# Optimization experiments

Measured on AMD Instinct MI355X. Metric: run time of the kernel, lower is better.

The kernel has to match this reference:

```python
import jax, jax.numpy as jnp
import numpy as np

L = 1024
D = 512      # d_model
H = 256      # hidden


def setup_inputs() -> dict:
    key = jax.random.key(0)
    k1, k2, k3, k4, k5 = jax.random.split(key, 5)
    scale = 0.02
    return {
        "seq_feats": jax.random.normal(k1, (L, D), dtype=jnp.float32),
        "W1": jax.random.normal(k2, (H, 2 * D), dtype=jnp.float32) * scale,
        "b1": jax.random.normal(k3, (H,), dtype=jnp.float32) * scale,
        "W2": jax.random.normal(k4, (1, H), dtype=jnp.float32) * scale,
        "b2": jax.random.normal(k5, (1,), dtype=jnp.float32) * scale,
    }


def reference(seq_feats, W1, b1, W2, b2):
    # cat([a, b]) @ W1.T == a @ W1[:, :D].T + b @ W1[:, D:].T
    # so we never materialize the [L, L, 2D] concat tensor.
    d = seq_feats.shape[1]
    pa = seq_feats @ W1[:, :d].T          # [L, H] (row / i contribution)
    pb = seq_feats @ W1[:, d:].T          # [L, H] (col / j contribution)
    h = jax.nn.relu(pa[:, None, :] + pb[None, :, :] + b1)  # [L, L, H]
    scores = jnp.einsum("ijh,h->ij", h, W2[0]) + b2[0]      # [L, L]
    scores = (scores + scores.T) * 0.5
    return jax.nn.sigmoid(scores)
```

## Files before the change

kernel.cpp:

```cpp
#include <hip/hip_runtime.h>
#include <hip/hip_bf16.h>
#include <math.h>

#define LL 1024
#define DD 512
#define HH 256

typedef __attribute__((ext_vector_type(8))) short bf16x8;
typedef __attribute__((ext_vector_type(4))) float f32x4;


__device__ __forceinline__ ushort f2bf(float f) {
  __hip_bfloat16 h = __float2bfloat16(f);
  return *reinterpret_cast<ushort*>(&h);
}
__device__ __forceinline__ float bfu(ushort u) {
  return __uint_as_float(((unsigned int)u) << 16);
}

__global__ __launch_bounds__(256) void sp_convert(
    const float* __restrict__ S, const float* __restrict__ W1,
    ushort* __restrict__ Sb, ushort* __restrict__ Wb) {
  const int m = blockIdx.x * 256 + threadIdx.x;
  const int NS = (LL * DD) / 4;
  if (m < NS) {
    const float4 v = ((const float4*)S)[m];
    ushort4 o;
    o.x = f2bf(v.x); o.y = f2bf(v.y); o.z = f2bf(v.z); o.w = f2bf(v.w);
    ((ushort4*)Sb)[m] = o;
  } else {
    const int w  = m - NS;
    const int n  = w >> 7;
    const int kg = w & 127;
    const float4 v = *(const float4*)(W1 + (size_t)(n & 255) * 1024 +
                                      (n >> 8) * 512 + 4 * kg);
    ushort4 o;
    o.x = f2bf(v.x); o.y = f2bf(v.y); o.z = f2bf(v.z); o.w = f2bf(v.w);
    *(ushort4*)(Wb + (size_t)n * 512 + 4 * kg) = o;
  }
}

__global__ __launch_bounds__(256) void sp_mgemm(
    const ushort* __restrict__ Wb, const ushort* __restrict__ Sb,
    const float* __restrict__ b1, ushort* __restrict__ O) {
  const int tid  = threadIdx.x;
  const int lane = tid & 63;
  const int wv   = tid >> 6;
  const int i0   = blockIdx.x * 32 + (wv >> 1) * 16;
  const int n0   = blockIdx.y * 32 + (wv & 1) * 16;
  const int lr   = lane & 15;
  const int lg   = lane >> 4;

  const ushort* ap = Wb + (size_t)(n0 + lr) * 512 + lg * 8;
  const ushort* bp = Sb + (size_t)(i0 + lr) * 512 + lg * 8;

  f32x4 acc = {0.f, 0.f, 0.f, 0.f};
  #pragma unroll
  for (int ks = 0; ks < 512; ks += 32) {
    const bf16x8 af = *(const bf16x8*)(ap + ks);
    const bf16x8 bf = *(const bf16x8*)(bp + ks);
    acc = __builtin_amdgcn_mfma_f32_16x16x32_bf16(af, bf, acc, 0, 0, 0);
  }

  const bool hasB = (n0 < 256);
  #pragma unroll
  for (int r = 0; r < 4; ++r) {
    const int n = n0 + lg * 4 + r;
    float v = acc[r];
    if (hasB) v += b1[n];
    O[(size_t)n * LL + i0 + lr] = f2bf(v);
  }
}

__global__ __launch_bounds__(512) void sp_pairwise(
    const ushort* __restrict__ O, const float* __restrict__ W2,
    float* __restrict__ pz) {
  __shared__ float Tl[128][72];
  __shared__ float Ul[128][72];
  __shared__ float PR[4][128];
  __shared__ float As[64], Bs[64];

  const int tid = threadIdx.x;
  const int tx  = tid & 15;
  const int ty  = tid >> 4;
  const int j0  = blockIdx.x * 64;
  const int i0  = blockIdx.y * 64;
  const int hz  = blockIdx.z * 128;

  #pragma unroll
  for (int q = 0; q < 4; ++q) {
    const int m = q * 512 + tid;
    const int hh = m >> 4;
    const int g4 = (m & 15) * 4;
    const ushort4 tv = *(const ushort4*)(O + (size_t)(hz + hh) * LL + i0 + g4);
    const ushort4 uv = *(const ushort4*)(O + (size_t)(HH + hz + hh) * LL + j0 + g4);
    *(float4*)&Tl[hh][g4] = make_float4(bfu(tv.x), bfu(tv.y), bfu(tv.z), bfu(tv.w));
    *(float4*)&Ul[hh][g4] = make_float4(bfu(uv.x), bfu(uv.y), bfu(uv.z), bfu(uv.w));
  }
  __syncthreads();

  {
    const int x = tid & 127, hs = tid >> 7;
    const float* pan = (x < 64) ? &Tl[0][x] : &Ul[0][x - 64];
    float p = 0.f;
    #pragma unroll 8
    for (int n = 0; n < 32; ++n) {
      const int hh = hs * 32 + n;
      p = fmaf(pan[hh * 72], W2[hz + hh], p);
    }
    PR[hs][x] = p;
  }
  __syncthreads();
  if (tid < 128) {
    const float s = PR[0][tid] + PR[1][tid] + PR[2][tid] + PR[3][tid];
    if (tid < 64) As[tid] = s; else Bs[tid - 64] = s;
  }
  __syncthreads();

  float a0[4] = {0.f, 0.f, 0.f, 0.f};
  float a1[4] = {0.f, 0.f, 0.f, 0.f};

  #pragma unroll 4
  for (int hh = 0; hh < 128; ++hh) {
    const float2 tv = *(const float2*)&Tl[hh][2 * ty];
    const float4 uv = *(const float4*)&Ul[hh][4 * tx];
    const float w = W2[hz + hh];
    a0[0] = fmaf(fabsf(tv.x + uv.x), w, a0[0]);
    a0[1] = fmaf(fabsf(tv.x + uv.y), w, a0[1]);
    a0[2] = fmaf(fabsf(tv.x + uv.z), w, a0[2]);
    a0[3] = fmaf(fabsf(tv.x + uv.w), w, a0[3]);
    a1[0] = fmaf(fabsf(tv.y + uv.x), w, a1[0]);
    a1[1] = fmaf(fabsf(tv.y + uv.y), w, a1[1]);
    a1[2] = fmaf(fabsf(tv.y + uv.z), w, a1[2]);
    a1[3] = fmaf(fabsf(tv.y + uv.w), w, a1[3]);
  }

  const float A0 = As[2 * ty], A1 = As[2 * ty + 1];
  const float B0 = Bs[4 * tx], B1 = Bs[4 * tx + 1];
  const float B2 = Bs[4 * tx + 2], B3 = Bs[4 * tx + 3];
  float* po = pz + (size_t)blockIdx.z * ((size_t)LL * LL)
                 + (size_t)(i0 + 2 * ty) * LL + j0 + 4 * tx;
  *(float4*)po = make_float4(a0[0] + A0 + B0, a0[1] + A0 + B1,
                             a0[2] + A0 + B2, a0[3] + A0 + B3);
  *(float4*)(po + LL) = make_float4(a1[0] + A1 + B0, a1[1] + A1 + B1,
                                    a1[2] + A1 + B2, a1[3] + A1 + B3);
}

__global__ __launch_bounds__(1024) void sp_symsig(
    const float* __restrict__ pz, const float* __restrict__ b2,
    float* __restrict__ out) {
  __shared__ float B[64][65];
  const int i0 = blockIdx.y * 64;
  const int j0 = blockIdx.x * 64;
  const int r  = threadIdx.x >> 4;
  const int g  = threadIdx.x & 15;
  const size_t L2 = (size_t)LL * LL;

  const float* pm = pz + (size_t)(j0 + r) * LL + i0 + 4 * g;
  const float4 m0 = *(const float4*)(pm);
  const float4 m1 = *(const float4*)(pm + L2);
  B[r][4 * g + 0] = m0.x + m1.x;
  B[r][4 * g + 1] = m0.y + m1.y;
  B[r][4 * g + 2] = m0.z + m1.z;
  B[r][4 * g + 3] = m0.w + m1.w;
  __syncthreads();

  const float* pd = pz + (size_t)(i0 + r) * LL + j0 + 4 * g;
  const float4 d0 = *(const float4*)(pd);
  const float4 d1 = *(const float4*)(pd + L2);
  const float bb = b2[0];
  float4 o;
  float x;
  x = 0.25f * (d0.x + d1.x + B[4 * g + 0][r]) + bb; o.x = 1.f / (1.f + expf(-x));
  x = 0.25f * (d0.y + d1.y + B[4 * g + 1][r]) + bb; o.y = 1.f / (1.f + expf(-x));
  x = 0.25f * (d0.z + d1.z + B[4 * g + 2][r]) + bb; o.z = 1.f / (1.f + expf(-x));
  x = 0.25f * (d0.w + d1.w + B[4 * g + 3][r]) + bb; o.w = 1.f / (1.f + expf(-x));
  *(float4*)(out + (size_t)(i0 + r) * LL + j0 + 4 * g) = o;
}

extern "C" void kernel_launch(void* const* d_in, const int* in_sizes, int n_in,
                              void* d_out, int out_size, void* d_ws, size_t ws_size,
                              hipStream_t stream) {
  const float* S  = (const float*)d_in[0];
  const float* W1 = (const float*)d_in[1];
  const float* b1 = (const float*)d_in[2];
  const float* W2 = (const float*)d_in[3];
  const float* b2 = (const float*)d_in[4];
  float* out = (float*)d_out;

  float* ws = (float*)d_ws;
  ushort* Sb = (ushort*)ws;
  ushort* Wb = (ushort*)(ws + 262144);
  ushort* O  = (ushort*)(ws + 393216);
  float*  pz = ws + 655360;

  hipLaunchKernelGGL(sp_convert, dim3(768), dim3(256), 0, stream,
                     S, W1, Sb, Wb);
  hipLaunchKernelGGL(sp_mgemm, dim3(32, 16), dim3(256), 0, stream,
                     Wb, Sb, b1, O);
  hipLaunchKernelGGL(sp_pairwise, dim3(16, 16, 2), dim3(512), 0, stream,
                     O, W2, pz);
  hipLaunchKernelGGL(sp_symsig, dim3(16, 16), dim3(1024), 0, stream,
                     pz, b2, out);
}
```

Measured before the change: 46.39 us.

## Use 4x4 register tiles, four-way hidden split, and bf16 partial scores

Each thread in the pairwise kernel now computes a 4x4 output tile, which gives more arithmetic per shared-memory load. The block shrinks to 256 threads and the hidden dimension is split four ways, so 1024 blocks run. Partial score planes are stored as bf16, keeping intermediate traffic unchanged despite twice as many partials. In exchange, the partial sums lose precision and the symmetrize kernel must read four planes.

New measurement: 45.22 us. 2.5% less time.

```diff
diff --git a/kernel.cpp b/kernel.cpp
--- a/kernel.cpp
+++ b/kernel.cpp
@@ -72,12 +72,12 @@
   }
 }
 
-__global__ __launch_bounds__(512) void sp_pairwise(
+__global__ __launch_bounds__(256, 4) void sp_pairwise(
     const ushort* __restrict__ O, const float* __restrict__ W2,
-    float* __restrict__ pz) {
-  __shared__ float Tl[128][72];
-  __shared__ float Ul[128][72];
-  __shared__ float PR[4][128];
+    ushort* __restrict__ pz) {
+  __shared__ float Tl[64][72];
+  __shared__ float Ul[64][72];
+  __shared__ float PR[2][128];
   __shared__ float As[64], Bs[64];
 
   const int tid = threadIdx.x;
@@ -85,11 +85,11 @@
   const int ty  = tid >> 4;
   const int j0  = blockIdx.x * 64;
   const int i0  = blockIdx.y * 64;
-  const int hz  = blockIdx.z * 128;
+  const int hz  = blockIdx.z * 64;
 
   #pragma unroll
   for (int q = 0; q < 4; ++q) {
-    const int m = q * 512 + tid;
+    const int m = q * 256 + tid;
     const int hh = m >> 4;
     const int g4 = (m & 15) * 4;
     const ushort4 tv = *(const ushort4*)(O + (size_t)(hz + hh) * LL + i0 + g4);
@@ -112,42 +112,44 @@
   }
   __syncthreads();
   if (tid < 128) {
-    const float s = PR[0][tid] + PR[1][tid] + PR[2][tid] + PR[3][tid];
+    const float s = PR[0][tid] + PR[1][tid];
     if (tid < 64) As[tid] = s; else Bs[tid - 64] = s;
   }
   __syncthreads();
 
-  float a0[4] = {0.f, 0.f, 0.f, 0.f};
-  float a1[4] = {0.f, 0.f, 0.f, 0.f};
+  float acc[4][4] = {{0.f}};
 
   #pragma unroll 4
-  for (int hh = 0; hh < 128; ++hh) {
-    const float2 tv = *(const float2*)&Tl[hh][2 * ty];
-    const float4 uv = *(const float4*)&Ul[hh][4 * tx];
+  for (int hh = 0; hh < 64; ++hh) {
+    const float4 tv4 = *(const float4*)&Tl[hh][4 * ty];
+    const float4 uv4 = *(const float4*)&Ul[hh][4 * tx];
     const float w = W2[hz + hh];
-    a0[0] = fmaf(fabsf(tv.x + uv.x), w, a0[0]);
-    a0[1] = fmaf(fabsf(tv.x + uv.y), w, a0[1]);
-    a0[2] = fmaf(fabsf(tv.x + uv.z), w, a0[2]);
-    a0[3] = fmaf(fabsf(tv.x + uv.w), w, a0[3]);
-    a1[0] = fmaf(fabsf(tv.y + uv.x), w, a1[0]);
-    a1[1] = fmaf(fabsf(tv.y + uv.y), w, a1[1]);
-    a1[2] = fmaf(fabsf(tv.y + uv.z), w, a1[2]);
-    a1[3] = fmaf(fabsf(tv.y + uv.w), w, a1[3]);
-  }
-
-  const float A0 = As[2 * ty], A1 = As[2 * ty + 1];
-  const float B0 = Bs[4 * tx], B1 = Bs[4 * tx + 1];
-  const float B2 = Bs[4 * tx + 2], B3 = Bs[4 * tx + 3];
-  float* po = pz + (size_t)blockIdx.z * ((size_t)LL * LL)
-                 + (size_t)(i0 + 2 * ty) * LL + j0 + 4 * tx;
-  *(float4*)po = make_float4(a0[0] + A0 + B0, a0[1] + A0 + B1,
-                             a0[2] + A0 + B2, a0[3] + A0 + B3);
-  *(float4*)(po + LL) = make_float4(a1[0] + A1 + B0, a1[1] + A1 + B1,
-                                    a1[2] + A1 + B2, a1[3] + A1 + B3);
+    const float tv[4] = {tv4.x, tv4.y, tv4.z, tv4.w};
+    const float uv[4] = {uv4.x, uv4.y, uv4.z, uv4.w};
+    #pragma unroll
+    for (int a = 0; a < 4; ++a) {
+      #pragma unroll
+      for (int b = 0; b < 4; ++b) {
+        acc[a][b] = fmaf(fabsf(tv[a] + uv[b]), w, acc[a][b]);
+      }
+    }
+  }
+
+  ushort* po = pz + (size_t)blockIdx.z * ((size_t)LL * LL);
+  #pragma unroll
+  for (int a = 0; a < 4; ++a) {
+    const float Ai = As[4 * ty + a];
+    ushort4 v;
+    v.x = f2bf(acc[a][0] + Ai + Bs[4 * tx + 0]);
+    v.y = f2bf(acc[a][1] + Ai + Bs[4 * tx + 1]);
+    v.z = f2bf(acc[a][2] + Ai + Bs[4 * tx + 2]);
+    v.w = f2bf(acc[a][3] + Ai + Bs[4 * tx + 3]);
+    *(ushort4*)(po + (size_t)(i0 + 4 * ty + a) * LL + j0 + 4 * tx) = v;
+  }
 }
 
 __global__ __launch_bounds__(1024) void sp_symsig(
-    const float* __restrict__ pz, const float* __restrict__ b2,
+    const ushort* __restrict__ pz, const float* __restrict__ b2,
     float* __restrict__ out) {
   __shared__ float B[64][65];
   const int i0 = blockIdx.y * 64;
@@ -156,25 +158,33 @@
   const int g  = threadIdx.x & 15;
   const size_t L2 = (size_t)LL * LL;
 
-  const float* pm = pz + (size_t)(j0 + r) * LL + i0 + 4 * g;
-  const float4 m0 = *(const float4*)(pm);
-  const float4 m1 = *(const float4*)(pm + L2);
-  B[r][4 * g + 0] = m0.x + m1.x;
-  B[r][4 * g + 1] = m0.y + m1.y;
-  B[r][4 * g + 2] = m0.z + m1.z;
-  B[r][4 * g + 3] = m0.w + m1.w;
-  __syncthreads();
-
-  const float* pd = pz + (size_t)(i0 + r) * LL + j0 + 4 * g;
-  const float4 d0 = *(const float4*)(pd);
-  const float4 d1 = *(const float4*)(pd + L2);
+  const ushort* pm = pz + (size_t)(j0 + r) * LL + i0 + 4 * g;
+  const ushort4 m0 = *(const ushort4*)(pm);
+  const ushort4 m1 = *(const ushort4*)(pm + L2);
+  const ushort4 m2 = *(const ushort4*)(pm + 2 * L2);
+  const ushort4 m3 = *(const ushort4*)(pm + 3 * L2);
+  B[r][4 * g + 0] = bfu(m0.x) + bfu(m1.x) + bfu(m2.x) + bfu(m3.x);
+  B[r][4 * g + 1] = bfu(m0.y) + bfu(m1.y) + bfu(m2.y) + bfu(m3.y);
+  B[r][4 * g + 2] = bfu(m0.z) + bfu(m1.z) + bfu(m2.z) + bfu(m3.z);
+  B[r][4 * g + 3] = bfu(m0.w) + bfu(m1.w) + bfu(m2.w) + bfu(m3.w);
+  __syncthreads();
+
+  const ushort* pd = pz + (size_t)(i0 + r) * LL + j0 + 4 * g;
+  const ushort4 d0 = *(const ushort4*)(pd);
+  const ushort4 d1 = *(const ushort4*)(pd + L2);
+  const ushort4 d2 = *(const ushort4*)(pd + 2 * L2);
+  const ushort4 d3 = *(const ushort4*)(pd + 3 * L2);
   const float bb = b2[0];
   float4 o;
   float x;
-  x = 0.25f * (d0.x + d1.x + B[4 * g + 0][r]) + bb; o.x = 1.f / (1.f + expf(-x));
-  x = 0.25f * (d0.y + d1.y + B[4 * g + 1][r]) + bb; o.y = 1.f / (1.f + expf(-x));
-  x = 0.25f * (d0.z + d1.z + B[4 * g + 2][r]) + bb; o.z = 1.f / (1.f + expf(-x));
-  x = 0.25f * (d0.w + d1.w + B[4 * g + 3][r]) + bb; o.w = 1.f / (1.f + expf(-x));
+  x = 0.25f * (bfu(d0.x) + bfu(d1.x) + bfu(d2.x) + bfu(d3.x) + B[4 * g + 0][r]) + bb;
+  o.x = 1.f / (1.f + expf(-x));
+  x = 0.25f * (bfu(d0.y) + bfu(d1.y) + bfu(d2.y) + bfu(d3.y) + B[4 * g + 1][r]) + bb;
+  o.y = 1.f / (1.f + expf(-x));
+  x = 0.25f * (bfu(d0.z) + bfu(d1.z) + bfu(d2.z) + bfu(d3.z) + B[4 * g + 2][r]) + bb;
+  o.z = 1.f / (1.f + expf(-x));
+  x = 0.25f * (bfu(d0.w) + bfu(d1.w) + bfu(d2.w) + bfu(d3.w) + B[4 * g + 3][r]) + bb;
+  o.w = 1.f / (1.f + expf(-x));
   *(float4*)(out + (size_t)(i0 + r) * LL + j0 + 4 * g) = o;
 }
 
@@ -192,13 +202,13 @@
   ushort* Sb = (ushort*)ws;
   ushort* Wb = (ushort*)(ws + 262144);
   ushort* O  = (ushort*)(ws + 393216);
-  float*  pz = ws + 655360;
+  ushort* pz = (ushort*)(ws + 655360);
 
   hipLaunchKernelGGL(sp_convert, dim3(768), dim3(256), 0, stream,
                      S, W1, Sb, Wb);
   hipLaunchKernelGGL(sp_mgemm, dim3(32, 16), dim3(256), 0, stream,
                      Wb, Sb, b1, O);
-  hipLaunchKernelGGL(sp_pairwise, dim3(16, 16, 2), dim3(512), 0, stream,
+  hipLaunchKernelGGL(sp_pairwise, dim3(16, 16, 4), dim3(256), 0, stream,
                      O, W2, pz);
   hipLaunchKernelGGL(sp_symsig, dim3(16, 16), dim3(1024), 0, stream,
                      pz, b2, out);
```
